# Optimization experiments

Hardware: AMD Instinct MI355X
Metric: run time of the kernel (lower is better)

## Reference

```python
import jax, jax.numpy as jnp
import numpy as np

N = 50000   # nodes
E = 800000  # edges
V = 10000   # vocab
D = 128     # emb_dim
H = 128     # hidden_dim
C = 10      # num_classes
G = 512     # graphs in batch


def setup_inputs() -> dict:
    key = jax.random.key(0)
    ks = jax.random.split(key, 10)
    return {
        "x_tokens": jax.random.randint(ks[0], (N,), 0, V),
        "edge_index": jax.random.randint(ks[1], (2, E), 0, N),
        "batch": jnp.sort(jax.random.randint(ks[2], (N,), 0, G)),
        "emb": jax.random.normal(ks[3], (V, D), dtype=jnp.float32) * 0.05,
        "w1": jax.random.normal(ks[4], (D, H), dtype=jnp.float32) * 0.05,
        "b1": jax.random.normal(ks[5], (H,), dtype=jnp.float32) * 0.05,
        "w2": jax.random.normal(ks[6], (H, H), dtype=jnp.float32) * 0.05,
        "b2": jax.random.normal(ks[7], (H,), dtype=jnp.float32) * 0.05,
        "lin_w": jax.random.normal(ks[8], (H, C), dtype=jnp.float32) * 0.05,
        "lin_b": jax.random.normal(ks[9], (C,), dtype=jnp.float32) * 0.05,
    }


def _gcn_conv(x, W, b, src, dst, norm):
    # PyG GCNConv: x' = D^{-1/2}(A+I)D^{-1/2} X W + b (self-loops already in src/dst)
    h = x @ W                                  # [N, H]
    msg = h[src] * norm[:, None]               # [E+N, H] gather + scale
    return jax.ops.segment_sum(msg, dst, num_segments=N) + b


def reference(x_tokens, edge_index, batch, emb, w1, b1, w2, b2, lin_w, lin_b):
    # embedding with padding_idx=0 (row 0 forced to zero)
    table = emb * (jnp.arange(V) != 0)[:, None].astype(emb.dtype)
    x = table[x_tokens]                        # [N, D]

    # add self loops, symmetric degree normalization (computed once)
    loops = jnp.arange(N)
    src = jnp.concatenate([edge_index[0], loops])
    dst = jnp.concatenate([edge_index[1], loops])
    deg = jax.ops.segment_sum(jnp.ones_like(dst, dtype=x.dtype), dst, num_segments=N)
    dis = jax.lax.rsqrt(deg)                   # deg >= 1 due to self loops
    norm = dis[src] * dis[dst]                 # [E+N]

    x = jax.nn.relu(_gcn_conv(x, w1, b1, src, dst, norm))
    x = jax.nn.relu(_gcn_conv(x, w2, b2, src, dst, norm))

    # global mean pool over graphs
    sums = jax.ops.segment_sum(x, batch, num_segments=G)          # [G, H]
    cnts = jax.ops.segment_sum(jnp.ones((N,), x.dtype), batch, num_segments=G)
    pooled = sums / jnp.maximum(cnts, 1.0)[:, None]

    return pooled @ lin_w + lin_b              # [G, C]
```

## Files before the change

kernel.cpp:

```cpp
#include <hip/hip_runtime.h>
#include <hip/hip_bf16.h>


typedef unsigned int uint;
typedef unsigned short ushort;
typedef __attribute__((ext_vector_type(8))) short bf16x8;
typedef __attribute__((ext_vector_type(4))) float f32x4;

__device__ inline float bf_lo(uint u) { return __uint_as_float(u << 16); }
__device__ inline float bf_hi(uint u) { return __uint_as_float(u & 0xffff0000u); }
__device__ inline float bf1(ushort u) { return __uint_as_float(((uint)u) << 16); }
__device__ inline ushort f2bf(float f) {
    uint u = __float_as_uint(f);
    return (ushort)((u + 0x7fffu + ((u >> 16) & 1u)) >> 16);
}
__device__ inline uint pack2bf(float a, float b) {
    return (uint)f2bf(a) | ((uint)f2bf(b) << 16);
}

#define EPB 2048
#define CAP 8192

__global__ __launch_bounds__(256) void init_kernel(int4* __restrict__ z, int n4) {
    int i = blockIdx.x * blockDim.x + threadIdx.x;
    if (i < n4) z[i] = make_int4(0, 0, 0, 0);
}

__global__ __launch_bounds__(256) void convert_w(const float* __restrict__ W1,
                                                 const float* __restrict__ W2,
                                                 ushort* __restrict__ W1t,
                                                 ushort* __restrict__ W2t) {
    int i = blockIdx.x * 256 + threadIdx.x;
    const float* Ws = (i < 16384) ? W1 : W2;
    ushort* Wd      = (i < 16384) ? W1t : W2t;
    int j = i & 16383;
    int nn = j >> 7, k = j & 127;
    Wd[j] = f2bf(Ws[k * 128 + nn]);
}

__global__ __launch_bounds__(256) void bucket_scatter(const int* __restrict__ src,
                                                      const int* __restrict__ dst,
                                                      int* __restrict__ bcur,
                                                      uint* __restrict__ bstage,
                                                      int E, int NB) {
    __shared__ int lh[256];
    __shared__ int lbase[257];
    __shared__ int gbase[256];
    __shared__ int lcur[256];
    __shared__ uint stage[EPB];
    const int t = threadIdx.x;
    const int base = blockIdx.x * EPB;
    const int end  = min(E, base + EPB);
    const int tot  = end - base;

    lh[t] = 0;
    __syncthreads();

    uint pk[8]; int bk[8]; int cnt = 0;
    for (int i = base + t; i < end; i += 256) {
        int s = src[i];
        uint d = (uint)dst[i];
        bk[cnt] = (int)(d >> 8);
        pk[cnt] = (uint)s | ((d & 255u) << 24);
        atomicAdd(&lh[bk[cnt]], 1);
        ++cnt;
    }
    __syncthreads();

    if (t < NB && lh[t]) gbase[t] = t * CAP + atomicAdd(&bcur[t], lh[t]);
    {
        __shared__ int ls[256];
        int v = lh[t];
        ls[t] = v;
        __syncthreads();
        for (int off = 1; off < 256; off <<= 1) {
            int x = (t >= off) ? ls[t - off] : 0;
            __syncthreads();
            ls[t] += x;
            __syncthreads();
        }
        lbase[t] = ls[t] - v;
        if (t == 255) lbase[256] = ls[255];
        lcur[t] = 0;
    }
    __syncthreads();

    for (int j = 0; j < cnt; ++j) {
        int p = lbase[bk[j]] + atomicAdd(&lcur[bk[j]], 1);
        stage[p] = pk[j];
    }
    __syncthreads();

    for (int i = t; i < tot; i += 256) {
        int lo = 0, hi = 256;
        while (lo + 1 < hi) {
            int mid = (lo + hi) >> 1;
            if (lbase[mid] <= i) lo = mid; else hi = mid;
        }
        bstage[gbase[lo] + (i - lbase[lo])] = stage[i];
    }
}

__global__ __launch_bounds__(256) void csr_build(const uint* __restrict__ bstage,
                                                 const int* __restrict__ bcur,
                                                 float* __restrict__ dis,
                                                 int* __restrict__ rbeg,
                                                 int* __restrict__ rend,
                                                 int* __restrict__ csr,
                                                 int N, int NB) {
    __shared__ int lh[256];
    __shared__ int ls[256];
    __shared__ int lbase[256];
    __shared__ int lcur[256];
    const int b = blockIdx.x;
    const int t = threadIdx.x;
    const int base  = b * CAP;
    const int cntb  = bcur[b];
    const int n0    = b << 8;
    const int nn    = min(256, N - n0);

    lh[t] = 0;
    __syncthreads();
    for (int i = t; i < cntb; i += 256)
        atomicAdd(&lh[bstage[base + i] >> 24], 1);
    __syncthreads();

    const int v = lh[t];
    ls[t] = v;
    __syncthreads();
    for (int off = 1; off < 256; off <<= 1) {
        int x = (t >= off) ? ls[t - off] : 0;
        __syncthreads();
        ls[t] += x;
        __syncthreads();
    }
    lbase[t] = ls[t] - v;
    lcur[t] = 0;
    if (t < nn) {
        dis[n0 + t]  = rsqrtf((float)v + 1.0f);
        rbeg[n0 + t] = base + lbase[t];
        rend[n0 + t] = base + lbase[t] + v;
    }
    __syncthreads();

    for (int i = t; i < cntb; i += 256) {
        uint e = bstage[base + i];
        int dl = (int)(e >> 24);
        int pos = base + lbase[dl] + atomicAdd(&lcur[dl], 1);
        csr[pos] = (int)(e & 0xFFFFFFu);
    }
}

template<bool GATHER>
__global__ __launch_bounds__(256) void gemm_mfma(const ushort* __restrict__ Xbf,
                                                 const int* __restrict__ tokens,
                                                 const float* __restrict__ emb,
                                                 const ushort* __restrict__ Wt,
                                                 ushort* __restrict__ Out, int n) {
    __shared__ ushort wl[128 * 128];
    const int tid = threadIdx.x;

    {
        const int row  = tid >> 1;
        const int half = tid & 1;
        const int base = row * 256 + half * 128;
#pragma unroll
        for (int i = 0; i < 8; ++i) {
            int off = base + i * 16;
            uint4 v = *(const uint4*)((const char*)Wt + off);
            int swz = off ^ ((row & 7) << 4);
            *(uint4*)((char*)wl + swz) = v;
        }
    }
    __syncthreads();

    const int w  = tid >> 6;
    const int l  = tid & 63;
    const int lr = l & 15;
    const int lg = l >> 4;
    const int rowBase = blockIdx.x * 128 + w * 32;

    f32x4 acc[2][8];
#pragma unroll
    for (int s = 0; s < 2; ++s)
#pragma unroll
        for (int ct = 0; ct < 8; ++ct) acc[s][ct] = (f32x4){0.f, 0.f, 0.f, 0.f};

    bf16x8 afrag[2][4];
#pragma unroll
    for (int s = 0; s < 2; ++s) {
        const int row = rowBase + s * 16 + lr;
        if (row < n) {
            if (GATHER) {
                const int tok = tokens[row];
                if (tok != 0) {
                    const float* ep = emb + (size_t)tok * 128;
#pragma unroll
                    for (int kk = 0; kk < 4; ++kk) {
                        const float* q = ep + kk * 32 + lg * 8;
                        float4 lo = *(const float4*)q;
                        float4 hi = *(const float4*)(q + 4);
                        uint4 pk;
                        pk.x = pack2bf(lo.x, lo.y); pk.y = pack2bf(lo.z, lo.w);
                        pk.z = pack2bf(hi.x, hi.y); pk.w = pack2bf(hi.z, hi.w);
                        union { uint4 u; bf16x8 b; } c; c.u = pk;
                        afrag[s][kk] = c.b;
                    }
                } else {
#pragma unroll
                    for (int kk = 0; kk < 4; ++kk) afrag[s][kk] = (bf16x8){0,0,0,0,0,0,0,0};
                }
            } else {
                const ushort* xp = Xbf + (size_t)row * 128;
#pragma unroll
                for (int kk = 0; kk < 4; ++kk)
                    afrag[s][kk] = *(const bf16x8*)(xp + kk * 32 + lg * 8);
            }
        } else {
#pragma unroll
            for (int kk = 0; kk < 4; ++kk) afrag[s][kk] = (bf16x8){0,0,0,0,0,0,0,0};
        }
    }

#pragma unroll
    for (int ct = 0; ct < 8; ++ct) {
#pragma unroll
        for (int kk = 0; kk < 4; ++kk) {
            const int nrow = ct * 16 + lr;
            int off = nrow * 256 + kk * 64 + lg * 16;
            off ^= ((nrow & 7) << 4);
            bf16x8 b = *(const bf16x8*)((const char*)wl + off);
            acc[0][ct] = __builtin_amdgcn_mfma_f32_16x16x32_bf16(afrag[0][kk], b, acc[0][ct], 0, 0, 0);
            acc[1][ct] = __builtin_amdgcn_mfma_f32_16x16x32_bf16(afrag[1][kk], b, acc[1][ct], 0, 0, 0);
        }
    }

#pragma unroll
    for (int s = 0; s < 2; ++s) {
#pragma unroll
        for (int r = 0; r < 4; ++r) {
            const int row = rowBase + s * 16 + lg * 4 + r;
            if (row < n) {
                ushort* op = Out + (size_t)row * 128 + lr;
#pragma unroll
                for (int ct = 0; ct < 8; ++ct)
                    op[ct * 16] = f2bf(acc[s][ct][r]);
            }
        }
    }
}

__global__ __launch_bounds__(256) void aggregate_kernel(const ushort* __restrict__ H,
                                                        const float* __restrict__ dis,
                                                        const int* __restrict__ rbeg,
                                                        const int* __restrict__ rend,
                                                        const int* __restrict__ csr,
                                                        const float* __restrict__ bias,
                                                        ushort* __restrict__ Out, int n) {
    const int g = threadIdx.x >> 4;
    const int l = threadIdx.x & 15;
    const int node = blockIdx.x * 16 + g;
    if (node >= n) return;

    const float dn = dis[node];
    const uint4 hq = *(const uint4*)(H + (size_t)node * 128 + l * 8);
    const int e0 = rbeg[node];
    const int e1 = rend[node];

    float s0_ = 0.f, s1_ = 0.f, s2_ = 0.f, s3_ = 0.f,
          s4_ = 0.f, s5_ = 0.f, s6_ = 0.f, s7_ = 0.f;

    int e = e0;
    for (; e + 8 <= e1; e += 8) {
        int a[8];
#pragma unroll
        for (int j = 0; j < 8; ++j) a[j] = csr[e + j];
        float w[8];
#pragma unroll
        for (int j = 0; j < 8; ++j) w[j] = dis[a[j]];
        uint4 h[8];
#pragma unroll
        for (int j = 0; j < 8; ++j) h[j] = *(const uint4*)(H + (size_t)a[j] * 128 + l * 8);
#pragma unroll
        for (int j = 0; j < 8; ++j) {
            s0_ += bf_lo(h[j].x) * w[j]; s1_ += bf_hi(h[j].x) * w[j];
            s2_ += bf_lo(h[j].y) * w[j]; s3_ += bf_hi(h[j].y) * w[j];
            s4_ += bf_lo(h[j].z) * w[j]; s5_ += bf_hi(h[j].z) * w[j];
            s6_ += bf_lo(h[j].w) * w[j]; s7_ += bf_hi(h[j].w) * w[j];
        }
    }
    for (; e + 4 <= e1; e += 4) {
        int a[4];
#pragma unroll
        for (int j = 0; j < 4; ++j) a[j] = csr[e + j];
        float w[4];
#pragma unroll
        for (int j = 0; j < 4; ++j) w[j] = dis[a[j]];
        uint4 h[4];
#pragma unroll
        for (int j = 0; j < 4; ++j) h[j] = *(const uint4*)(H + (size_t)a[j] * 128 + l * 8);
#pragma unroll
        for (int j = 0; j < 4; ++j) {
            s0_ += bf_lo(h[j].x) * w[j]; s1_ += bf_hi(h[j].x) * w[j];
            s2_ += bf_lo(h[j].y) * w[j]; s3_ += bf_hi(h[j].y) * w[j];
            s4_ += bf_lo(h[j].z) * w[j]; s5_ += bf_hi(h[j].z) * w[j];
            s6_ += bf_lo(h[j].w) * w[j]; s7_ += bf_hi(h[j].w) * w[j];
        }
    }
    for (; e < e1; ++e) {
        const int a = csr[e];
        const float w = dis[a];
        const uint4 h = *(const uint4*)(H + (size_t)a * 128 + l * 8);
        s0_ += bf_lo(h.x)*w; s1_ += bf_hi(h.x)*w;
        s2_ += bf_lo(h.y)*w; s3_ += bf_hi(h.y)*w;
        s4_ += bf_lo(h.z)*w; s5_ += bf_hi(h.z)*w;
        s6_ += bf_lo(h.w)*w; s7_ += bf_hi(h.w)*w;
    }

    const float self = dn * dn;
    const float4 bA = *(const float4*)&bias[l * 8];
    const float4 bB = *(const float4*)&bias[l * 8 + 4];
    float o0 = fmaxf(s0_ * dn + bf_lo(hq.x) * self + bA.x, 0.0f);
    float o1 = fmaxf(s1_ * dn + bf_hi(hq.x) * self + bA.y, 0.0f);
    float o2 = fmaxf(s2_ * dn + bf_lo(hq.y) * self + bA.z, 0.0f);
    float o3 = fmaxf(s3_ * dn + bf_hi(hq.y) * self + bA.w, 0.0f);
    float o4 = fmaxf(s4_ * dn + bf_lo(hq.z) * self + bB.x, 0.0f);
    float o5 = fmaxf(s5_ * dn + bf_hi(hq.z) * self + bB.y, 0.0f);
    float o6 = fmaxf(s6_ * dn + bf_lo(hq.w) * self + bB.z, 0.0f);
    float o7 = fmaxf(s7_ * dn + bf_hi(hq.w) * self + bB.w, 0.0f);

    uint4 o;
    o.x = pack2bf(o0, o1); o.y = pack2bf(o2, o3);
    o.z = pack2bf(o4, o5); o.w = pack2bf(o6, o7);
    *(uint4*)(Out + (size_t)node * 128 + l * 8) = o;
}

__global__ __launch_bounds__(256) void pool_partial(const ushort* __restrict__ X,
                                                    const int* __restrict__ batch,
                                                    float* __restrict__ pooled,
                                                    int* __restrict__ gcnt, int n) {
    const int grp = threadIdx.x >> 7;
    const int t   = threadIdx.x & 127;
    const int r0  = blockIdx.x * 128 + grp * 64;
    if (r0 >= n) return;
    const int r1 = min(r0 + 64, n);

    int gcur = batch[r0];
    float sum = 0.0f;
    int cnt = 0;
    for (int r = r0; r < r1; ++r) {
        const int g = batch[r];
        const float v = bf1(X[(size_t)r * 128 + t]);
        if (g != gcur) {
            atomicAdd(&pooled[(size_t)gcur * 128 + t], sum);
            if (t == 0) atomicAdd(&gcnt[gcur], cnt);
            sum = 0.0f; cnt = 0; gcur = g;
        }
        sum += v; ++cnt;
    }
    atomicAdd(&pooled[(size_t)gcur * 128 + t], sum);
    if (t == 0) atomicAdd(&gcnt[gcur], cnt);
}

__global__ __launch_bounds__(128) void pool_finalize(const float* __restrict__ pooled,
                                                     const int* __restrict__ gcnt,
                                                     const float* __restrict__ lw,
                                                     const float* __restrict__ lb,
                                                     float* __restrict__ out) {
    const int g = blockIdx.x;
    const int t = threadIdx.x;
    __shared__ float pl[128];
    const float c = fmaxf((float)gcnt[g], 1.0f);
    pl[t] = pooled[(size_t)g * 128 + t] / c;
    __syncthreads();
    if (t < 10) {
        float acc = lb[t];
#pragma unroll 16
        for (int d = 0; d < 128; ++d) acc += pl[d] * lw[d * 10 + t];
        out[g * 10 + t] = acc;
    }
}

extern "C" void kernel_launch(void* const* d_in, const int* in_sizes, int n_in,
                              void* d_out, int out_size, void* d_ws, size_t ws_size,
                              hipStream_t stream) {
    const int*   tokens = (const int*)d_in[0];
    const int*   eidx   = (const int*)d_in[1];
    const int*   batch  = (const int*)d_in[2];
    const float* emb    = (const float*)d_in[3];
    const float* w1     = (const float*)d_in[4];
    const float* b1     = (const float*)d_in[5];
    const float* w2     = (const float*)d_in[6];
    const float* b2     = (const float*)d_in[7];
    const float* lw     = (const float*)d_in[8];
    const float* lbv    = (const float*)d_in[9];

    const int N = in_sizes[0];
    const int E = in_sizes[1] / 2;
    const int G = out_size / 10;
    const int* src = eidx;
    const int* dst = eidx + E;
    const int NB = (N + 255) >> 8;

    char* p = (char*)d_ws;
    auto alloc = [&](size_t bytes) { void* r = (void*)p; p += (bytes + 255) & ~(size_t)255; return r; };
    float*  dis    = (float*)alloc((size_t)N * 4);
    int*    rbeg   = (int*)  alloc((size_t)N * 4);
    int*    rend   = (int*)  alloc((size_t)N * 4);
    int*    zreg   = (int*)  alloc((size_t)(768 + (size_t)G * 128) * 4);
    int*    bcur   = zreg;
    int*    gcnt   = zreg + 256;
    float*  pooled = (float*)(zreg + 768);
    uint*   bstage = (uint*) alloc((size_t)NB * CAP * 4);
    int*    csr    = (int*)  alloc((size_t)NB * CAP * 4);
    ushort* W1t    = (ushort*)alloc(16384 * 2);
    ushort* W2t    = (ushort*)alloc(16384 * 2);
    ushort* A      = (ushort*)alloc((size_t)N * 128 * 2);
    ushort* B      = (ushort*)alloc((size_t)N * 128 * 2);

    const int ZN4 = (768 + G * 128) / 4;
    const int EB  = (E + EPB - 1) / EPB;

    init_kernel   <<<(ZN4 + 255) / 256, 256, 0, stream>>>((int4*)zreg, ZN4);
    convert_w     <<<128, 256, 0, stream>>>(w1, w2, W1t, W2t);
    bucket_scatter<<<EB, 256, 0, stream>>>(src, dst, bcur, bstage, E, NB);
    csr_build     <<<NB, 256, 0, stream>>>(bstage, bcur, dis, rbeg, rend, csr, N, NB);

    gemm_mfma<true><<<(N + 127) / 128, 256, 0, stream>>>(nullptr, tokens, emb, W1t, A, N);
    aggregate_kernel<<<(N + 15) / 16, 256, 0, stream>>>(A, dis, rbeg, rend, csr, b1, B, N);

    gemm_mfma<false><<<(N + 127) / 128, 256, 0, stream>>>(B, nullptr, nullptr, W2t, A, N);
    aggregate_kernel<<<(N + 15) / 16, 256, 0, stream>>>(A, dis, rbeg, rend, csr, b2, B, N);

    pool_partial <<<(N + 127) / 128, 256, 0, stream>>>(B, batch, pooled, gcnt, N);
    pool_finalize<<<G, 128, 0, stream>>>(pooled, gcnt, lw, lbv, (float*)d_out);
}
```

Measured before the change: 155.1 us.

## Pre-scale GEMM output by source norm, fuse pooling into second aggregation

```diff
diff --git a/kernel.cpp b/kernel.cpp
--- a/kernel.cpp
+++ b/kernel.cpp
@@ -9,7 +9,6 @@
 
 __device__ inline float bf_lo(uint u) { return __uint_as_float(u << 16); }
 __device__ inline float bf_hi(uint u) { return __uint_as_float(u & 0xffff0000u); }
-__device__ inline float bf1(ushort u) { return __uint_as_float(((uint)u) << 16); }
 __device__ inline ushort f2bf(float f) {
     uint u = __float_as_uint(f);
     return (ushort)((u + 0x7fffu + ((u >> 16) & 1u)) >> 16);
@@ -21,21 +20,23 @@
 #define EPB 2048
 #define CAP 8192
 
-__global__ __launch_bounds__(256) void init_kernel(int4* __restrict__ z, int n4) {
-    int i = blockIdx.x * blockDim.x + threadIdx.x;
-    if (i < n4) z[i] = make_int4(0, 0, 0, 0);
-}
-
-__global__ __launch_bounds__(256) void convert_w(const float* __restrict__ W1,
-                                                 const float* __restrict__ W2,
-                                                 ushort* __restrict__ W1t,
-                                                 ushort* __restrict__ W2t) {
-    int i = blockIdx.x * 256 + threadIdx.x;
-    const float* Ws = (i < 16384) ? W1 : W2;
-    ushort* Wd      = (i < 16384) ? W1t : W2t;
-    int j = i & 16383;
-    int nn = j >> 7, k = j & 127;
-    Wd[j] = f2bf(Ws[k * 128 + nn]);
+__global__ __launch_bounds__(256) void init_convert(int4* __restrict__ z, int n4,
+                                                    const float* __restrict__ W1,
+                                                    const float* __restrict__ W2,
+                                                    ushort* __restrict__ W1t,
+                                                    ushort* __restrict__ W2t) {
+    const int zb = (n4 + 255) >> 8;
+    if ((int)blockIdx.x < zb) {
+        int i = blockIdx.x * 256 + threadIdx.x;
+        if (i < n4) z[i] = make_int4(0, 0, 0, 0);
+    } else {
+        int i = (blockIdx.x - zb) * 256 + threadIdx.x;
+        const float* Ws = (i < 16384) ? W1 : W2;
+        ushort* Wd      = (i < 16384) ? W1t : W2t;
+        int j = i & 16383;
+        int nn = j >> 7, k = j & 127;
+        Wd[j] = f2bf(Ws[k * 128 + nn]);
+    }
 }
 
 __global__ __launch_bounds__(256) void bucket_scatter(const int* __restrict__ src,
@@ -156,6 +157,7 @@
                                                  const int* __restrict__ tokens,
                                                  const float* __restrict__ emb,
                                                  const ushort* __restrict__ Wt,
+                                                 const float* __restrict__ dis,
                                                  ushort* __restrict__ Out, int n) {
     __shared__ ushort wl[128 * 128];
     const int tid = threadIdx.x;
@@ -241,136 +243,150 @@
         for (int r = 0; r < 4; ++r) {
             const int row = rowBase + s * 16 + lg * 4 + r;
             if (row < n) {
+                const float sc = dis[row];
                 ushort* op = Out + (size_t)row * 128 + lr;
 #pragma unroll
                 for (int ct = 0; ct < 8; ++ct)
-                    op[ct * 16] = f2bf(acc[s][ct][r]);
+                    op[ct * 16] = f2bf(acc[s][ct][r] * sc);
             }
         }
     }
 }
 
+template<bool FUSE_POOL>
 __global__ __launch_bounds__(256) void aggregate_kernel(const ushort* __restrict__ H,
                                                         const float* __restrict__ dis,
                                                         const int* __restrict__ rbeg,
                                                         const int* __restrict__ rend,
                                                         const int* __restrict__ csr,
                                                         const float* __restrict__ bias,
-                                                        ushort* __restrict__ Out, int n) {
+                                                        ushort* __restrict__ Out,
+                                                        const int* __restrict__ batch,
+                                                        float* __restrict__ pooled,
+                                                        int n) {
     const int g = threadIdx.x >> 4;
     const int l = threadIdx.x & 15;
     const int node = blockIdx.x * 16 + g;
-    if (node >= n) return;
-
-    const float dn = dis[node];
-    const uint4 hq = *(const uint4*)(H + (size_t)node * 128 + l * 8);
-    const int e0 = rbeg[node];
-    const int e1 = rend[node];
-
-    float s0_ = 0.f, s1_ = 0.f, s2_ = 0.f, s3_ = 0.f,
-          s4_ = 0.f, s5_ = 0.f, s6_ = 0.f, s7_ = 0.f;
-
-    int e = e0;
-    for (; e + 8 <= e1; e += 8) {
-        int a[8];
-#pragma unroll
-        for (int j = 0; j < 8; ++j) a[j] = csr[e + j];
-        float w[8];
-#pragma unroll
-        for (int j = 0; j < 8; ++j) w[j] = dis[a[j]];
-        uint4 h[8];
-#pragma unroll
-        for (int j = 0; j < 8; ++j) h[j] = *(const uint4*)(H + (size_t)a[j] * 128 + l * 8);
-#pragma unroll
-        for (int j = 0; j < 8; ++j) {
-            s0_ += bf_lo(h[j].x) * w[j]; s1_ += bf_hi(h[j].x) * w[j];
-            s2_ += bf_lo(h[j].y) * w[j]; s3_ += bf_hi(h[j].y) * w[j];
-            s4_ += bf_lo(h[j].z) * w[j]; s5_ += bf_hi(h[j].z) * w[j];
-            s6_ += bf_lo(h[j].w) * w[j]; s7_ += bf_hi(h[j].w) * w[j];
-        }
-    }
-    for (; e + 4 <= e1; e += 4) {
-        int a[4];
-#pragma unroll
-        for (int j = 0; j < 4; ++j) a[j] = csr[e + j];
-        float w[4];
-#pragma unroll
-        for (int j = 0; j < 4; ++j) w[j] = dis[a[j]];
-        uint4 h[4];
-#pragma unroll
-        for (int j = 0; j < 4; ++j) h[j] = *(const uint4*)(H + (size_t)a[j] * 128 + l * 8);
-#pragma unroll
-        for (int j = 0; j < 4; ++j) {
-            s0_ += bf_lo(h[j].x) * w[j]; s1_ += bf_hi(h[j].x) * w[j];
-            s2_ += bf_lo(h[j].y) * w[j]; s3_ += bf_hi(h[j].y) * w[j];
-            s4_ += bf_lo(h[j].z) * w[j]; s5_ += bf_hi(h[j].z) * w[j];
-            s6_ += bf_lo(h[j].w) * w[j]; s7_ += bf_hi(h[j].w) * w[j];
-        }
-    }
-    for (; e < e1; ++e) {
-        const int a = csr[e];
-        const float w = dis[a];
-        const uint4 h = *(const uint4*)(H + (size_t)a * 128 + l * 8);
-        s0_ += bf_lo(h.x)*w; s1_ += bf_hi(h.x)*w;
-        s2_ += bf_lo(h.y)*w; s3_ += bf_hi(h.y)*w;
-        s4_ += bf_lo(h.z)*w; s5_ += bf_hi(h.z)*w;
-        s6_ += bf_lo(h.w)*w; s7_ += bf_hi(h.w)*w;
-    }
-
-    const float self = dn * dn;
+    const bool valid = node < n;
+
+    float s0_=0.f,s1_=0.f,s2_=0.f,s3_=0.f,s4_=0.f,s5_=0.f,s6_=0.f,s7_=0.f;
+    float dn = 0.f;
     const float4 bA = *(const float4*)&bias[l * 8];
     const float4 bB = *(const float4*)&bias[l * 8 + 4];
-    float o0 = fmaxf(s0_ * dn + bf_lo(hq.x) * self + bA.x, 0.0f);
-    float o1 = fmaxf(s1_ * dn + bf_hi(hq.x) * self + bA.y, 0.0f);
-    float o2 = fmaxf(s2_ * dn + bf_lo(hq.y) * self + bA.z, 0.0f);
-    float o3 = fmaxf(s3_ * dn + bf_hi(hq.y) * self + bA.w, 0.0f);
-    float o4 = fmaxf(s4_ * dn + bf_lo(hq.z) * self + bB.x, 0.0f);
-    float o5 = fmaxf(s5_ * dn + bf_hi(hq.z) * self + bB.y, 0.0f);
-    float o6 = fmaxf(s6_ * dn + bf_lo(hq.w) * self + bB.z, 0.0f);
-    float o7 = fmaxf(s7_ * dn + bf_hi(hq.w) * self + bB.w, 0.0f);
-
-    uint4 o;
-    o.x = pack2bf(o0, o1); o.y = pack2bf(o2, o3);
-    o.z = pack2bf(o4, o5); o.w = pack2bf(o6, o7);
-    *(uint4*)(Out + (size_t)node * 128 + l * 8) = o;
-}
-
-__global__ __launch_bounds__(256) void pool_partial(const ushort* __restrict__ X,
-                                                    const int* __restrict__ batch,
-                                                    float* __restrict__ pooled,
-                                                    int* __restrict__ gcnt, int n) {
-    const int grp = threadIdx.x >> 7;
-    const int t   = threadIdx.x & 127;
-    const int r0  = blockIdx.x * 128 + grp * 64;
-    if (r0 >= n) return;
-    const int r1 = min(r0 + 64, n);
-
-    int gcur = batch[r0];
-    float sum = 0.0f;
-    int cnt = 0;
-    for (int r = r0; r < r1; ++r) {
-        const int g = batch[r];
-        const float v = bf1(X[(size_t)r * 128 + t]);
-        if (g != gcur) {
-            atomicAdd(&pooled[(size_t)gcur * 128 + t], sum);
-            if (t == 0) atomicAdd(&gcnt[gcur], cnt);
-            sum = 0.0f; cnt = 0; gcur = g;
-        }
-        sum += v; ++cnt;
-    }
-    atomicAdd(&pooled[(size_t)gcur * 128 + t], sum);
-    if (t == 0) atomicAdd(&gcnt[gcur], cnt);
+
+    if (valid) {
+        dn = dis[node];
+        const uint4 hq = *(const uint4*)(H + (size_t)node * 128 + l * 8);
+        s0_ = bf_lo(hq.x); s1_ = bf_hi(hq.x);
+        s2_ = bf_lo(hq.y); s3_ = bf_hi(hq.y);
+        s4_ = bf_lo(hq.z); s5_ = bf_hi(hq.z);
+        s6_ = bf_lo(hq.w); s7_ = bf_hi(hq.w);
+
+        const int e0 = rbeg[node];
+        const int e1 = rend[node];
+        int e = e0;
+        for (; e + 8 <= e1; e += 8) {
+            int a[8];
+#pragma unroll
+            for (int j = 0; j < 8; ++j) a[j] = csr[e + j];
+            uint4 h[8];
+#pragma unroll
+            for (int j = 0; j < 8; ++j) h[j] = *(const uint4*)(H + (size_t)a[j] * 128 + l * 8);
+#pragma unroll
+            for (int j = 0; j < 8; ++j) {
+                s0_ += bf_lo(h[j].x); s1_ += bf_hi(h[j].x);
+                s2_ += bf_lo(h[j].y); s3_ += bf_hi(h[j].y);
+                s4_ += bf_lo(h[j].z); s5_ += bf_hi(h[j].z);
+                s6_ += bf_lo(h[j].w); s7_ += bf_hi(h[j].w);
+            }
+        }
+        for (; e + 4 <= e1; e += 4) {
+            int a[4];
+#pragma unroll
+            for (int j = 0; j < 4; ++j) a[j] = csr[e + j];
+            uint4 h[4];
+#pragma unroll
+            for (int j = 0; j < 4; ++j) h[j] = *(const uint4*)(H + (size_t)a[j] * 128 + l * 8);
+#pragma unroll
+            for (int j = 0; j < 4; ++j) {
+                s0_ += bf_lo(h[j].x); s1_ += bf_hi(h[j].x);
+                s2_ += bf_lo(h[j].y); s3_ += bf_hi(h[j].y);
+                s4_ += bf_lo(h[j].z); s5_ += bf_hi(h[j].z);
+                s6_ += bf_lo(h[j].w); s7_ += bf_hi(h[j].w);
+            }
+        }
+        for (; e < e1; ++e) {
+            const uint4 h = *(const uint4*)(H + (size_t)csr[e] * 128 + l * 8);
+            s0_ += bf_lo(h.x); s1_ += bf_hi(h.x);
+            s2_ += bf_lo(h.y); s3_ += bf_hi(h.y);
+            s4_ += bf_lo(h.z); s5_ += bf_hi(h.z);
+            s6_ += bf_lo(h.w); s7_ += bf_hi(h.w);
+        }
+    }
+
+    const float o0 = fmaxf(s0_ * dn + bA.x, 0.0f);
+    const float o1 = fmaxf(s1_ * dn + bA.y, 0.0f);
+    const float o2 = fmaxf(s2_ * dn + bA.z, 0.0f);
+    const float o3 = fmaxf(s3_ * dn + bA.w, 0.0f);
+    const float o4 = fmaxf(s4_ * dn + bB.x, 0.0f);
+    const float o5 = fmaxf(s5_ * dn + bB.y, 0.0f);
+    const float o6 = fmaxf(s6_ * dn + bB.z, 0.0f);
+    const float o7 = fmaxf(s7_ * dn + bB.w, 0.0f);
+
+    if constexpr (!FUSE_POOL) {
+        if (valid) {
+            uint4 o;
+            o.x = pack2bf(o0, o1); o.y = pack2bf(o2, o3);
+            o.z = pack2bf(o4, o5); o.w = pack2bf(o6, o7);
+            *(uint4*)(Out + (size_t)node * 128 + l * 8) = o;
+        }
+    } else {
+        __shared__ float x3[16][128];
+        __shared__ int bv[16];
+        if (valid) {
+            float4 va, vb;
+            va.x = o0; va.y = o1; va.z = o2; va.w = o3;
+            vb.x = o4; vb.y = o5; vb.z = o6; vb.w = o7;
+            *(float4*)&x3[g][l * 8]     = va;
+            *(float4*)&x3[g][l * 8 + 4] = vb;
+            if (l == 0) bv[g] = batch[node];
+        } else if (l == 0) {
+            bv[g] = -1;
+        }
+        __syncthreads();
+        const int t = threadIdx.x;
+        if (t < 128) {
+            int cur = bv[0];
+            float run = 0.0f;
+            for (int r = 0; r < 16; ++r) {
+                const int b = bv[r];
+                if (b < 0) break;
+                if (b != cur) {
+                    if (run != 0.0f) atomicAdd(&pooled[(size_t)cur * 128 + t], run);
+                    cur = b; run = 0.0f;
+                }
+                run += x3[r][t];
+            }
+            if (cur >= 0 && run != 0.0f) atomicAdd(&pooled[(size_t)cur * 128 + t], run);
+        }
+    }
 }
 
 __global__ __launch_bounds__(128) void pool_finalize(const float* __restrict__ pooled,
-                                                     const int* __restrict__ gcnt,
+                                                     const int* __restrict__ batch,
                                                      const float* __restrict__ lw,
                                                      const float* __restrict__ lb,
-                                                     float* __restrict__ out) {
+                                                     float* __restrict__ out, int n) {
     const int g = blockIdx.x;
     const int t = threadIdx.x;
+    int lo = 0, hi = n;
+    while (lo < hi) { int mid = (lo + hi) >> 1; if (batch[mid] < g) lo = mid + 1; else hi = mid; }
+    const int s = lo;
+    hi = n;
+    while (lo < hi) { int mid = (lo + hi) >> 1; if (batch[mid] < g + 1) lo = mid + 1; else hi = mid; }
+    const float c = fmaxf((float)(lo - s), 1.0f);
+
     __shared__ float pl[128];
-    const float c = fmaxf((float)gcnt[g], 1.0f);
     pl[t] = pooled[(size_t)g * 128 + t] / c;
     __syncthreads();
     if (t < 10) {
@@ -407,10 +423,9 @@
     float*  dis    = (float*)alloc((size_t)N * 4);
     int*    rbeg   = (int*)  alloc((size_t)N * 4);
     int*    rend   = (int*)  alloc((size_t)N * 4);
-    int*    zreg   = (int*)  alloc((size_t)(768 + (size_t)G * 128) * 4);
+    int*    zreg   = (int*)  alloc((size_t)(256 + (size_t)G * 128) * 4);
     int*    bcur   = zreg;
-    int*    gcnt   = zreg + 256;
-    float*  pooled = (float*)(zreg + 768);
+    float*  pooled = (float*)(zreg + 256);
     uint*   bstage = (uint*) alloc((size_t)NB * CAP * 4);
     int*    csr    = (int*)  alloc((size_t)NB * CAP * 4);
     ushort* W1t    = (ushort*)alloc(16384 * 2);
@@ -418,20 +433,19 @@
     ushort* A      = (ushort*)alloc((size_t)N * 128 * 2);
     ushort* B      = (ushort*)alloc((size_t)N * 128 * 2);
 
-    const int ZN4 = (768 + G * 128) / 4;
+    const int ZN4 = (256 + G * 128) / 4;
+    const int ZB  = (ZN4 + 255) / 256;
     const int EB  = (E + EPB - 1) / EPB;
 
-    init_kernel   <<<(ZN4 + 255) / 256, 256, 0, stream>>>((int4*)zreg, ZN4);
-    convert_w     <<<128, 256, 0, stream>>>(w1, w2, W1t, W2t);
+    init_convert  <<<ZB + 128, 256, 0, stream>>>((int4*)zreg, ZN4, w1, w2, W1t, W2t);
     bucket_scatter<<<EB, 256, 0, stream>>>(src, dst, bcur, bstage, E, NB);
     csr_build     <<<NB, 256, 0, stream>>>(bstage, bcur, dis, rbeg, rend, csr, N, NB);
 
-    gemm_mfma<true><<<(N + 127) / 128, 256, 0, stream>>>(nullptr, tokens, emb, W1t, A, N);
-    aggregate_kernel<<<(N + 15) / 16, 256, 0, stream>>>(A, dis, rbeg, rend, csr, b1, B, N);
-
-    gemm_mfma<false><<<(N + 127) / 128, 256, 0, stream>>>(B, nullptr, nullptr, W2t, A, N);
-    aggregate_kernel<<<(N + 15) / 16, 256, 0, stream>>>(A, dis, rbeg, rend, csr, b2, B, N);
-
-    pool_partial <<<(N + 127) / 128, 256, 0, stream>>>(B, batch, pooled, gcnt, N);
-    pool_finalize<<<G, 128, 0, stream>>>(pooled, gcnt, lw, lbv, (float*)d_out);
-}
+    gemm_mfma<true><<<(N + 127) / 128, 256, 0, stream>>>(nullptr, tokens, emb, W1t, dis, A, N);
+    aggregate_kernel<false><<<(N + 15) / 16, 256, 0, stream>>>(A, dis, rbeg, rend, csr, b1, B, nullptr, nullptr, N);
+
+    gemm_mfma<false><<<(N + 127) / 128, 256, 0, stream>>>(B, nullptr, nullptr, W2t, dis, A, N);
+    aggregate_kernel<true><<<(N + 15) / 16, 256, 0, stream>>>(A, dis, rbeg, rend, csr, b2, nullptr, batch, pooled, N);
+
+    pool_finalize<<<G, 128, 0, stream>>>(pooled, batch, lw, lbv, (float*)d_out, N);
+}
```

New measurement: 142.6 us. 8.0% less time.
